# Performance work log

Measured on AMD Instinct MI355X. Metric: run time of the kernel, lower is better.

The kernel has to match this reference:

```python
import jax, jax.numpy as jnp
import numpy as np

B, T, I, H, L, O = 8192, 204, 5, 24, 10, 612

def setup_inputs() -> dict:
    key = jax.random.key(0)
    ks = jax.random.split(key, 10)
    s_ih = 1.0 / np.sqrt(H)
    inp = {
        "x": jax.random.normal(ks[0], (B, T, I), dtype=jnp.float32),
        # torch nn.LSTM params: weight_ih_l0 [4H,I], weight_hh_l0 [4H,H], biases [4H]
        "W_ih": jax.random.uniform(ks[1], (4 * H, I), jnp.float32, -s_ih, s_ih),
        "W_hh": jax.random.uniform(ks[2], (4 * H, H), jnp.float32, -s_ih, s_ih),
        "b_ih": jax.random.uniform(ks[3], (4 * H,), jnp.float32, -s_ih, s_ih),
        "b_hh": jax.random.uniform(ks[4], (4 * H,), jnp.float32, -s_ih, s_ih),
        "fc0_w": jax.random.uniform(ks[5], (L, H * T), jnp.float32, -1 / np.sqrt(H * T), 1 / np.sqrt(H * T)),
        "fc0_b": jax.random.uniform(ks[6], (L,), jnp.float32, -1 / np.sqrt(H * T), 1 / np.sqrt(H * T)),
        "out_w": jax.random.uniform(ks[7], (O, L), jnp.float32, -1 / np.sqrt(L), 1 / np.sqrt(L)),
        "out_b": jax.random.uniform(ks[8], (O,), jnp.float32, -1 / np.sqrt(L), 1 / np.sqrt(L)),
    }
    return inp

def _lstm_forward(x, W_ih, W_hh, b_ih, b_hh):
    # Precompute input projections for all timesteps: [B,T,4H] -> time-major [T,B,4H]
    x_proj = jnp.einsum("bti,gi->btg", x, W_ih) + b_ih
    x_proj = jnp.swapaxes(x_proj, 0, 1)
    h0 = jnp.zeros((x.shape[0], W_hh.shape[1]), x.dtype)
    c0 = jnp.zeros_like(h0)

    def step(carry, xt):
        h, c = carry
        gates = xt + h @ W_hh.T + b_hh  # [B,4H]; torch gate order i,f,g,o
        i, f, g, o = jnp.split(gates, 4, axis=-1)
        c = jax.nn.sigmoid(f) * c + jax.nn.sigmoid(i) * jnp.tanh(g)
        h = jax.nn.sigmoid(o) * jnp.tanh(c)
        return (h, c), h

    _, hs = jax.lax.scan(step, (h0, c0), x_proj)  # hs: [T,B,H]
    return jnp.swapaxes(hs, 0, 1)  # [B,T,H]

def reference(x, W_ih, W_hh, b_ih, b_hh, fc0_w, fc0_b, out_w, out_b):
    h = _lstm_forward(x, W_ih, W_hh, b_ih, b_hh)       # [B,T,H]
    h = h.reshape(h.shape[0], -1)                       # [B, T*H]
    h = jax.nn.relu(h @ fc0_w.T + fc0_b)                # [B, L]
    return h @ out_w.T + out_b                          # [B, O]
```

## Files before the change

### kernel.cpp

```cpp
#include <hip/hip_runtime.h>
#include <math.h>

#define T_  204
#define I_  5
#define H_  24
#define L_  10
#define O_  612
#define Bsz 8192

typedef _Float16 half8 __attribute__((ext_vector_type(8)));
typedef _Float16 half2t __attribute__((ext_vector_type(2)));
typedef float    float4t __attribute__((ext_vector_type(4)));

union U16B { float4t f4; half8 h8; float f[4]; _Float16 h[8]; half2t h2[4]; };

__device__ __forceinline__ float fast_rcp(float x){ return __builtin_amdgcn_rcpf(x); }
__device__ __forceinline__ float fast_ex2(float x){ return __builtin_amdgcn_exp2f(x); }
__device__ __forceinline__ half2t pk2(float a, float b){
    return __builtin_bit_cast(half2t, __builtin_amdgcn_cvt_pkrtz(a, b));
}

#define MFMA16(a,b,c) __builtin_amdgcn_mfma_f32_16x16x32_f16((a),(b),(c),0,0,0)

#define L2E  1.44269504f
#define L2E2 2.88539008f

__device__ __forceinline__ int unit_of(int q, int T) {
    return (q < 3) ? (8*q + T) : (8*(T >> 1) + 6 + (T & 1));
}

__global__ __launch_bounds__(64)
void pack_fc0(const float* __restrict__ fc0_w, float4t* __restrict__ dst)
{
    const int t = blockIdx.x, lane = threadIdx.x;
    const int m = lane & 15, q = lane >> 4;
    U16B v;
    #pragma unroll
    for (int i = 0; i < 8; ++i) {
        const int k = 8*q + i;
        float f = (m < L_ && k < H_) ? fc0_w[m*(T_*H_) + t*H_ + k] : 0.0f;
        v.h[i] = (_Float16)f;
    }
    dst[t*64 + lane] = v.f4;
}

#define ACT1(Dv, cc, hh)                                                        \
  {                                                                             \
    const float ei = fast_ex2((Dv)[0] * -L2E);                                  \
    const float ef = fast_ex2((Dv)[1] * -L2E);                                  \
    const float eg = fast_ex2((Dv)[2] *  L2E2);                                 \
    const float eo = fast_ex2((Dv)[3] * -L2E);                                  \
    const float Dn1 = 1.f + ef;                                                 \
    const float Dn2 = 1.f + ei;                                                 \
    const float Dn3 = eg + 1.f;                                                 \
    const float G   = eg - 1.f;                                                 \
    const float P   = Dn2 * Dn3;                                                \
    const float R1  = fast_rcp(Dn1 * P);                                        \
    const float nm  = fmaf((cc), P, Dn1 * G);                                   \
    (cc) = nm * R1;                                                             \
    const float es  = fast_ex2(__builtin_fabsf(cc) * -L2E2);                    \
    const float R2  = fast_rcp((1.f + eo) * (1.f + es));                        \
    (hh) = __builtin_copysignf((1.f - es) * R2, (cc));                          \
  }

#define POS(K, faK, xsK)                                                        \
  {                                                                             \
    float4t D0 = MFMA16(Ag[0], B.h8, zf4);                                      \
    float4t D1 = MFMA16(Ag[1], B.h8, zf4);                                      \
    float4t D2 = MFMA16(Ag[2], B.h8, zf4);                                      \
    float4t D3 = MFMA16(Ag[3], B.h8, zf4);                                      \
    float4t D4 = MFMA16(Ag[4], B.h8, zf4);                                      \
    float4t D5 = MFMA16(Ag[5], B.h8, zf4);                                      \
    const float4t E0 = mhi ? D3 : D0;                                           \
    const float4t E1 = mhi ? D4 : D1;                                           \
    const float4t E2 = mhi ? D5 : D2;                                           \
    float h0, h1, h2;                                                           \
    ACT1(E0, c0, h0)                                                            \
    ACT1(E1, c1, h1)                                                            \
    ACT1(E2, c2, h2)                                                            \
      \
    const float s0 = __shfl(h0, sPart, 64);                                     \
    const float s1 = __shfl(h1, sPart, 64);                                     \
    const float s2 = __shfl(h2, sPart, 64);                                     \
    const float rA = __shfl(h0, srcA, 64);                                      \
    const float rB = __shfl(h1, srcB, 64);                                      \
    const float rC = __shfl(h2, srcC, 64);                                      \
    if (q < 3) {                                                                \
         \
      B.h2[0] = pk2(mhi ? s0 : h0, mhi ? s1 : h1);                              \
      B.h2[1] = pk2(mhi ? s2 : h2, mhi ? h0 : s0);                              \
      B.h2[2] = pk2(mhi ? h1 : s1, mhi ? h2 : s2);                              \
       \
       \
      const float pa = (q == 0) ? rA : ((q == 1) ? rC : rB);                    \
      const float pb = (q == 0) ? rB : ((q == 1) ? rA : rC);                    \
      B.h2[3] = pk2(pa, pb);                                                    \
    } else {                                                                    \
      B.h2[0] = pk2(xsK[0], xsK[1]);                                            \
      B.h2[1] = pk2(xsK[2], xsK[3]);                                            \
      B.h2[2] = pk2(xsK[4], 1.0f);                                              \
      B.h2[3] = pk2(0.f, 0.f);                                                  \
    }                                                                           \
    { U16B fF; fF.f4 = faK;                                                     \
      accF = MFMA16(fF.h8, B.h8, accF); }                                       \
          \
    { const int tf = (t + K + 4 < T_) ? t + K + 4 : T_ - 1;                     \
      faK = fc0A[tf*64 + lane]; }                                               \
    if (q == 3) {                                                               \
      const int txi = (t + K + 5 < T_) ? t + K + 5 : T_ - 1;                    \
      const float* xq = xp + txi*I_;                                            \
      _Pragma("unroll")                                                         \
      for (int i = 0; i < I_; ++i) xsK[i] = xq[i];                              \
    }                                                                           \
  }

__global__ __launch_bounds__(64)
void lstm_mfma(const float* __restrict__ x,
               const float* __restrict__ W_ih,
               const float* __restrict__ W_hh,
               const float* __restrict__ b_ih,
               const float* __restrict__ b_hh,
               const float* __restrict__ fc0_b,
               const float* __restrict__ out_w,
               const float* __restrict__ out_b,
               const float4t* __restrict__ fc0A,
               float* __restrict__ out)
{
    __shared__ __align__(16) _Float16 actL[16*24];

    const int lane = threadIdx.x;
    const int m = lane & 15;
    const int q = lane >> 4;
    const int mb = m & 7;
    const bool mhi = (m >= 8);
    const int eb = blockIdx.x * 8 + mb;

    const int sPart = lane ^ 8;
    const int srcA = ((q == 1) ? 56 : 48) + mb;
    const int srcB = ((q == 2) ? 56 : 48) + mb;
    const int srcC = ((q == 2) ? 56 : 48) + mb;

    const float4t zf4 = {0.f, 0.f, 0.f, 0.f};

    half8 Ag[6];
    #pragma unroll
    for (int T6 = 0; T6 < 6; ++T6) {
        const int u = unit_of(m >> 2, T6);
        const int srow = (m & 3) * H_ + u;
        float wv[8];
        if (q < 3) {
            const float4t* pw = (const float4t*)(W_hh + srow*H_ + 8*q);
            float4t wa = pw[0], wb = pw[1];
            #pragma unroll
            for (int i = 0; i < 4; ++i) { wv[i] = wa[i]; wv[4+i] = wb[i]; }
        } else {
            #pragma unroll
            for (int i = 0; i < 8; ++i) wv[i] = 0.f;
            #pragma unroll
            for (int i = 0; i < I_; ++i) wv[i] = W_ih[srow*I_ + i];
            wv[5] = b_ih[srow] + b_hh[srow];
        }
        U16B tw;
        #pragma unroll
        for (int i = 0; i < 8; ++i) tw.h[i] = (_Float16)wv[i];
        Ag[T6] = tw.h8;
    }

    const float* xp = x + (size_t)eb * (T_*I_);

    U16B B;
    if (q == 3) {
        B.h2[0] = pk2(xp[0], xp[1]);
        B.h2[1] = pk2(xp[2], xp[3]);
        B.h2[2] = pk2(xp[4], 1.0f);
        B.h2[3] = pk2(0.f, 0.f);
    } else {
        B.f4 = zf4;
    }

    float4t fa0 = fc0A[0*64 + lane];
    float4t fa1 = fc0A[1*64 + lane];
    float4t fa2 = fc0A[2*64 + lane];
    float4t fa3 = fc0A[3*64 + lane];
    float xs0[I_] = {0,0,0,0,0}, xs1[I_] = {0,0,0,0,0};
    float xs2[I_] = {0,0,0,0,0}, xs3[I_] = {0,0,0,0,0};
    if (q == 3) {
        #pragma unroll
        for (int i = 0; i < I_; ++i) {
            xs0[i] = xp[1*I_ + i];
            xs1[i] = xp[2*I_ + i];
            xs2[i] = xp[3*I_ + i];
            xs3[i] = xp[4*I_ + i];
        }
    }

    float c0 = 0.f, c1 = 0.f, c2 = 0.f;
    float4t accF = zf4;

    #pragma unroll 1
    for (int t = 0; t < T_; t += 4) {
        POS(0, fa0, xs0)
        POS(1, fa1, xs1)
        POS(2, fa2, xs2)
        POS(3, fa3, xs3)
    }

    float av[4];
    #pragma unroll
    for (int r = 0; r < 4; ++r) {
        const int l = 4*q + r;
        const float fb = (l < L_) ? fc0_b[l] : 0.f;
        const float v = accF[r] + fb;
        av[r] = (l < L_) ? fmaxf(v, 0.f) : 0.f;
    }
    *(half2t*)(&actL[m*24 + 4*q])     = pk2(av[0], av[1]);
    *(half2t*)(&actL[m*24 + 4*q + 2]) = pk2(av[2], av[3]);
    __builtin_amdgcn_wave_barrier();

    U16B Ba;
    if (q < 2) Ba.f4 = *(const float4t*)(&actL[m*24 + q*8]);
    else       Ba.f4 = zf4;

    for (int Tt = 0; Tt < 39; ++Tt) {
        const int row = 16*Tt + m;
        float w0=0.f,w1=0.f,w2=0.f,w3=0.f,w4=0.f,w5=0.f,w6=0.f,w7=0.f;
        if (row < O_ && q < 2) {
            const float2* p2 = (const float2*)(out_w + row*L_);
            if (q == 0) {
                float2 a = p2[0], b = p2[1], cc = p2[2], dd = p2[3];
                w0=a.x; w1=a.y; w2=b.x; w3=b.y; w4=cc.x; w5=cc.y; w6=dd.x; w7=dd.y;
            } else {
                float2 a = p2[4];
                w0=a.x; w1=a.y;
            }
        }
        U16B Aw;
        Aw.h2[0] = pk2(w0,w1); Aw.h2[1] = pk2(w2,w3);
        Aw.h2[2] = pk2(w4,w5); Aw.h2[3] = pk2(w6,w7);

        float4t dd = MFMA16(Aw.h8, Ba.h8, zf4);

        const int ob = 16*Tt + 4*q;
        if (ob < O_ && m < 8) {
            const float4t bias = *(const float4t*)(out_b + ob);
            #pragma unroll
            for (int r = 0; r < 4; ++r) dd[r] += bias[r];
            *(float4t*)(out + (size_t)eb*O_ + ob) = dd;
        }
    }
}

extern "C" void kernel_launch(void* const* d_in, const int* in_sizes, int n_in,
                              void* d_out, int out_size, void* d_ws, size_t ws_size,
                              hipStream_t stream)
{
    const float* x     = (const float*)d_in[0];
    const float* W_ih  = (const float*)d_in[1];
    const float* W_hh  = (const float*)d_in[2];
    const float* b_ih  = (const float*)d_in[3];
    const float* b_hh  = (const float*)d_in[4];
    const float* fc0_w = (const float*)d_in[5];
    const float* fc0_b = (const float*)d_in[6];
    const float* out_w = (const float*)d_in[7];
    const float* out_b = (const float*)d_in[8];
    float* out = (float*)d_out;
    (void)ws_size;

    pack_fc0<<<dim3(T_), dim3(64), 0, stream>>>(fc0_w, (float4t*)d_ws);
    lstm_mfma<<<dim3(Bsz/8), dim3(64), 0, stream>>>(
        x, W_ih, W_hh, b_ih, b_hh, fc0_b, out_w, out_b,
        (const float4t*)d_ws, out);
}
```

Baseline: 195.2 us.

## Remap LSTM hidden units to 8 MFMA tiles and exchange h via DPP

Changes how the 24 hidden units map onto MFMA output rows. The recurrent step now issues 8 MFMAs instead of 6, and each lane evaluates 4 activation groups instead of 3, with rows 12-15 zero-padded. In exchange, the six cross-lane __shfl operations and their select logic become two fp16-packed DPP row-xor-8 moves plus simple selects. The cost of the extra MFMAs and activation math is traded against lower latency for the h redistribution on the serial time-step critical path. Launch bounds also add a minimum of one block.

```diff
diff --git a/kernel.cpp b/kernel.cpp
--- a/kernel.cpp
+++ b/kernel.cpp
@@ -19,15 +19,16 @@
 __device__ __forceinline__ half2t pk2(float a, float b){
     return __builtin_bit_cast(half2t, __builtin_amdgcn_cvt_pkrtz(a, b));
 }
+__device__ __forceinline__ float dpp_xor8(float v){
+    const int r = __builtin_amdgcn_mov_dpp(__builtin_bit_cast(int, v),
+                                           0x128 , 0xf, 0xf, true);
+    return __builtin_bit_cast(float, r);
+}
 
 #define MFMA16(a,b,c) __builtin_amdgcn_mfma_f32_16x16x32_f16((a),(b),(c),0,0,0)
 
 #define L2E  1.44269504f
 #define L2E2 2.88539008f
-
-__device__ __forceinline__ int unit_of(int q, int T) {
-    return (q < 3) ? (8*q + T) : (8*(T >> 1) + 6 + (T & 1));
-}
 
 __global__ __launch_bounds__(64)
 void pack_fc0(const float* __restrict__ fc0_w, float4t* __restrict__ dst)
@@ -71,30 +72,28 @@
     float4t D3 = MFMA16(Ag[3], B.h8, zf4);                                      \
     float4t D4 = MFMA16(Ag[4], B.h8, zf4);                                      \
     float4t D5 = MFMA16(Ag[5], B.h8, zf4);                                      \
-    const float4t E0 = mhi ? D3 : D0;                                           \
-    const float4t E1 = mhi ? D4 : D1;                                           \
-    const float4t E2 = mhi ? D5 : D2;                                           \
-    float h0, h1, h2;                                                           \
+    float4t D6 = MFMA16(Ag[6], B.h8, zf4);                                      \
+    float4t D7 = MFMA16(Ag[7], B.h8, zf4);                                      \
+    const float4t E0 = mhi ? D4 : D0;                                           \
+    const float4t E1 = mhi ? D5 : D1;                                           \
+    const float4t E2 = mhi ? D6 : D2;                                           \
+    const float4t E3 = mhi ? D7 : D3;                                           \
+    float h0, h1, h2, h3;                                                       \
     ACT1(E0, c0, h0)                                                            \
     ACT1(E1, c1, h1)                                                            \
     ACT1(E2, c2, h2)                                                            \
-      \
-    const float s0 = __shfl(h0, sPart, 64);                                     \
-    const float s1 = __shfl(h1, sPart, 64);                                     \
-    const float s2 = __shfl(h2, sPart, 64);                                     \
-    const float rA = __shfl(h0, srcA, 64);                                      \
-    const float rB = __shfl(h1, srcB, 64);                                      \
-    const float rC = __shfl(h2, srcC, 64);                                      \
+    ACT1(E3, c3, h3)                                                            \
+        \
+    const float pA = __builtin_bit_cast(float, pk2(h0, h1));                    \
+    const float pB = __builtin_bit_cast(float, pk2(h2, h3));                    \
+    const float rA = dpp_xor8(pA);                                              \
+    const float rB = dpp_xor8(pB);                                              \
     if (q < 3) {                                                                \
-         \
-      B.h2[0] = pk2(mhi ? s0 : h0, mhi ? s1 : h1);                              \
-      B.h2[1] = pk2(mhi ? s2 : h2, mhi ? h0 : s0);                              \
-      B.h2[2] = pk2(mhi ? h1 : s1, mhi ? h2 : s2);                              \
-       \
-       \
-      const float pa = (q == 0) ? rA : ((q == 1) ? rC : rB);                    \
-      const float pb = (q == 0) ? rB : ((q == 1) ? rA : rC);                    \
-      B.h2[3] = pk2(pa, pb);                                                    \
+           \
+      B.h2[0] = __builtin_bit_cast(half2t, mhi ? rA : pA);                      \
+      B.h2[1] = __builtin_bit_cast(half2t, mhi ? rB : pB);                      \
+      B.h2[2] = __builtin_bit_cast(half2t, mhi ? pA : rA);                      \
+      B.h2[3] = __builtin_bit_cast(half2t, mhi ? pB : rB);                      \
     } else {                                                                    \
       B.h2[0] = pk2(xsK[0], xsK[1]);                                            \
       B.h2[1] = pk2(xsK[2], xsK[3]);                                            \
@@ -114,7 +113,7 @@
     }                                                                           \
   }
 
-__global__ __launch_bounds__(64)
+__global__ __launch_bounds__(64, 1)
 void lstm_mfma(const float* __restrict__ x,
                const float* __restrict__ W_ih,
                const float* __restrict__ W_hh,
@@ -135,35 +134,34 @@
     const bool mhi = (m >= 8);
     const int eb = blockIdx.x * 8 + mb;
 
-    const int sPart = lane ^ 8;
-    const int srcA = ((q == 1) ? 56 : 48) + mb;
-    const int srcB = ((q == 2) ? 56 : 48) + mb;
-    const int srcC = ((q == 2) ? 56 : 48) + mb;
-
     const float4t zf4 = {0.f, 0.f, 0.f, 0.f};
 
-    half8 Ag[6];
+    half8 Ag[8];
     #pragma unroll
-    for (int T6 = 0; T6 < 6; ++T6) {
-        const int u = unit_of(m >> 2, T6);
-        const int srow = (m & 3) * H_ + u;
-        float wv[8];
-        if (q < 3) {
-            const float4t* pw = (const float4t*)(W_hh + srow*H_ + 8*q);
-            float4t wa = pw[0], wb = pw[1];
+    for (int T8 = 0; T8 < 8; ++T8) {
+        U16B tw;
+        if (m < 12) {
+            const int u = 8*(m >> 2) + T8;
+            const int srow = (m & 3) * H_ + u;
+            float wv[8];
+            if (q < 3) {
+                const float4t* pw = (const float4t*)(W_hh + srow*H_ + 8*q);
+                float4t wa = pw[0], wb = pw[1];
+                #pragma unroll
+                for (int i = 0; i < 4; ++i) { wv[i] = wa[i]; wv[4+i] = wb[i]; }
+            } else {
+                #pragma unroll
+                for (int i = 0; i < 8; ++i) wv[i] = 0.f;
+                #pragma unroll
+                for (int i = 0; i < I_; ++i) wv[i] = W_ih[srow*I_ + i];
+                wv[5] = b_ih[srow] + b_hh[srow];
+            }
             #pragma unroll
-            for (int i = 0; i < 4; ++i) { wv[i] = wa[i]; wv[4+i] = wb[i]; }
+            for (int i = 0; i < 8; ++i) tw.h[i] = (_Float16)wv[i];
         } else {
-            #pragma unroll
-            for (int i = 0; i < 8; ++i) wv[i] = 0.f;
-            #pragma unroll
-            for (int i = 0; i < I_; ++i) wv[i] = W_ih[srow*I_ + i];
-            wv[5] = b_ih[srow] + b_hh[srow];
-        }
-        U16B tw;
-        #pragma unroll
-        for (int i = 0; i < 8; ++i) tw.h[i] = (_Float16)wv[i];
-        Ag[T6] = tw.h8;
+            tw.f4 = zf4;
+        }
+        Ag[T8] = tw.h8;
     }
 
     const float* xp = x + (size_t)eb * (T_*I_);
@@ -194,7 +192,7 @@
         }
     }
 
-    float c0 = 0.f, c1 = 0.f, c2 = 0.f;
+    float c0 = 0.f, c1 = 0.f, c2 = 0.f, c3 = 0.f;
     float4t accF = zf4;
 
     #pragma unroll 1
```

New measurement: 204.4 us. 4.7% more time.
